# Optimization experiments

Hardware: AMD Instinct MI355X
Metric: run time of the kernel (lower is better)

The kernel has to match this reference:

```python
import jax, jax.numpy as jnp
import numpy as np

N_NODES = 50000
N_EDGES = 800000
N_GRAPHS = 256
NEG_SLOPE = 0.2

def selu(x):
    return jax.nn.selu(x)

def gat_conv(x, src, dst, W, att_l, att_r, b, n_nodes):
    """PyG GATConv, heads=1, with self-loops already appended to (src, dst).
    Message j->i: alpha_ij = softmax_i(leaky_relu(a_l.h_j + a_r.h_i)); out_i = sum_j alpha_ij h_j + b."""
    h = x @ W                                   # [N, C]
    a_src = h @ att_l                           # [N]
    a_dst = h @ att_r                           # [N]
    e = jax.nn.leaky_relu(a_src[src] + a_dst[dst], NEG_SLOPE)   # [E]
    # segment softmax over incoming edges of each dst node
    m = jax.ops.segment_max(e, dst, num_segments=n_nodes)       # [N]
    m = jnp.where(jnp.isfinite(m), m, 0.0)
    ex = jnp.exp(e - m[dst])
    denom = jax.ops.segment_sum(ex, dst, num_segments=n_nodes)  # [N]
    alpha = ex / jnp.maximum(denom, 1e-16)[dst]                  # [E]
    out = jax.ops.segment_sum(h[src] * alpha[:, None], dst, num_segments=n_nodes)
    return out + b

def global_mean_pool(x, batch, n_graphs):
    s = jax.ops.segment_sum(x, batch, num_segments=n_graphs)
    cnt = jax.ops.segment_sum(jnp.ones((x.shape[0],), x.dtype), batch, num_segments=n_graphs)
    return s / jnp.maximum(cnt, 1.0)[:, None]

def setup_inputs() -> dict:
    key = jax.random.key(0)
    ks = jax.random.split(key, 12)
    F_in, C, H, NC = 310, 256, 128, 2
    x = jax.random.normal(ks[0], (N_NODES, F_in), dtype=jnp.float32)
    edge_index = jax.random.randint(ks[1], (2, N_EDGES), 0, N_NODES, dtype=jnp.int64)
    batch = jnp.sort(jax.random.randint(ks[2], (N_NODES,), 0, N_GRAPHS, dtype=jnp.int64))
    g = lambda k, shp: jax.random.normal(k, shp, dtype=jnp.float32) * 0.05
    return {
        "x": x, "edge_index": edge_index, "batch": batch,
        "W1": g(ks[3], (F_in, C)), "att_l1": g(ks[4], (C,)), "att_r1": g(ks[5], (C,)),
        "b1": jnp.zeros((C,), jnp.float32),
        "W2": g(ks[6], (C, C)), "att_l2": g(ks[7], (C,)), "att_r2": g(ks[8], (C,)),
        "b2": jnp.zeros((C,), jnp.float32),
        "fc1_W": g(ks[9], (C, H)), "fc1_b": jnp.zeros((H,), jnp.float32),
        "fc2_W": g(ks[10], (H, NC)), "fc2_b": jnp.zeros((NC,), jnp.float32),
    }

def reference(x, edge_index, batch, W1, att_l1, att_r1, b1, W2, att_l2, att_r2, b2,
              fc1_W, fc1_b, fc2_W, fc2_b):
    n = x.shape[0]
    loops = jnp.arange(n, dtype=edge_index.dtype)
    src = jnp.concatenate([edge_index[0], loops])   # add_self_loops=True (PyG default)
    dst = jnp.concatenate([edge_index[1], loops])
    h = selu(gat_conv(x, src, dst, W1, att_l1, att_r1, b1, n))
    h = selu(gat_conv(h, src, dst, W2, att_l2, att_r2, b2, n))
    g = selu(global_mean_pool(h, batch, N_GRAPHS))      # [G, 256]
    g = selu(g @ fc1_W + fc1_b)                         # [G, 128]
    # dropout is identity in eval mode
    return jax.nn.log_softmax(g @ fc2_W + fc2_b, axis=-1)  # [G, 2]
```

## Files before the change

kernel.cpp:

```cpp
#include <hip/hip_runtime.h>
#include <hip/hip_bf16.h>

#define N_NODES 50000
#define N_EDGES 800000
#define N_TOT   (N_EDGES + N_NODES)
#define N_GRAPHS 256
#define F_IN 310
#define KP1 320
#define CH 256
#define HID 128
#define DEG_CAP 128

typedef __attribute__((ext_vector_type(8))) short short8;
typedef __attribute__((ext_vector_type(4))) float f32x4;
typedef unsigned short ushort_t;

__device__ __forceinline__ float selu_f(float x) {
    const float scale = 1.0507009873554805f;
    const float alpha = 1.6732632423543772f;
    return x > 0.f ? scale * x : scale * alpha * (expm1f(x));
}

__device__ __forceinline__ ushort_t f32_to_bf16_rne(float f) {
    unsigned u = __float_as_uint(f);
    unsigned rounding = 0x7FFFu + ((u >> 16) & 1u);
    return (ushort_t)((u + rounding) >> 16);
}
__device__ __forceinline__ float bf16_to_f32(ushort_t v) {
    return __uint_as_float(((unsigned)v) << 16);
}

__global__ __launch_bounds__(256) void convert_pad_x(
        const float* __restrict__ x, ushort_t* __restrict__ A) {
    int i = blockIdx.x * 256 + threadIdx.x;
    if (i >= N_NODES * (KP1 / 2)) return;
    int r = i / (KP1 / 2);
    int c2 = i - r * (KP1 / 2);
    int c = c2 * 2;
    ushort2 o = {0, 0};
    if (c2 < F_IN / 2) {
        float2 v = *(const float2*)(x + (long)r * F_IN + c);
        o.x = f32_to_bf16_rne(v.x);
        o.y = f32_to_bf16_rne(v.y);
    }
    *(ushort2*)(A + (long)r * KP1 + c) = o;
}

__global__ __launch_bounds__(256) void convert_wt(
        const float* __restrict__ W, ushort_t* __restrict__ Wt, int K, int Kp) {
    int i = blockIdx.x * blockDim.x + threadIdx.x;
    if (i >= CH * Kp) return;
    int n = i / Kp, k = i % Kp;
    Wt[i] = (k < K) ? f32_to_bf16_rne(W[(long)k * CH + n]) : 0;
}

__global__ __launch_bounds__(512) void gemm_bf16_fused(
        const ushort_t* __restrict__ A, const ushort_t* __restrict__ Bt,
        ushort_t* __restrict__ Cb, const float* __restrict__ att_l,
        const float* __restrict__ att_r, float* __restrict__ a_src,
        float* __restrict__ a_dst, int M, int Kp) {
    __shared__ __align__(16) ushort_t As[2][128 * 32];
    __shared__ __align__(16) ushort_t Bs[2][256 * 32];
    int tid = threadIdx.x;
    int row0 = blockIdx.x * 128;
    int w = tid >> 6, l = tid & 63;
    int lr = l & 15, lc = l >> 4;
    f32x4 acc[16] = {};

    int srow = l >> 2;
    int schunk = l & 3;
    int trowA = w * 16 + srow;
    int sx = schunk ^ (srow & 3);
    int garow = row0 + trowA; if (garow >= M) garow = M - 1;
    const ushort_t* gA  = A  + (size_t)garow * Kp + sx * 8;
    const ushort_t* gB0 = Bt + (size_t)trowA * Kp + sx * 8;
    const ushort_t* gB1 = Bt + (size_t)(128 + trowA) * Kp + sx * 8;
    int nt = Kp >> 5;

    auto stage = [&](int sel, int k0) {
        __builtin_amdgcn_global_load_lds(
            (const __attribute__((address_space(1))) void*)(gA + k0),
            (__attribute__((address_space(3))) void*)(&As[sel][w * 16 * 32]), 16, 0, 0);
        __builtin_amdgcn_global_load_lds(
            (const __attribute__((address_space(1))) void*)(gB0 + k0),
            (__attribute__((address_space(3))) void*)(&Bs[sel][w * 16 * 32]), 16, 0, 0);
        __builtin_amdgcn_global_load_lds(
            (const __attribute__((address_space(1))) void*)(gB1 + k0),
            (__attribute__((address_space(3))) void*)(&Bs[sel][(128 + w * 16) * 32]), 16, 0, 0);
    };

    stage(0, 0);
    __syncthreads();
    int cur = 0;
    for (int t = 0; t < nt; ++t) {
        if (t + 1 < nt) stage(cur ^ 1, (t + 1) << 5);
        int rA = w * 16 + lr;
        short8 af = *(const short8*)(&As[cur][rA * 32 + ((lc ^ (rA & 3)) * 8)]);
#pragma unroll
        for (int hn = 0; hn < 2; ++hn) {
            short8 bf[8];
#pragma unroll
            for (int nj = 0; nj < 8; ++nj) {
                int r = (hn * 8 + nj) * 16 + lr;
                bf[nj] = *(const short8*)(&Bs[cur][r * 32 + ((lc ^ (r & 3)) * 8)]);
            }
#pragma unroll
            for (int nj = 0; nj < 8; ++nj)
                acc[hn * 8 + nj] = __builtin_amdgcn_mfma_f32_16x16x32_bf16(
                    af, bf[nj], acc[hn * 8 + nj], 0, 0, 0);
        }
        __syncthreads();
        cur ^= 1;
    }

    float al[16], ar[16];
#pragma unroll
    for (int ni = 0; ni < 16; ++ni) {
        int col = ni * 16 + lr;
        al[ni] = att_l[col];
        ar[ni] = att_r[col];
    }
    int rbase = row0 + w * 16 + lc * 4;
#pragma unroll
    for (int q = 0; q < 4; ++q) {
        int grow = rbase + q;
        float pl = 0.f, pr = 0.f;
#pragma unroll
        for (int ni = 0; ni < 16; ++ni) {
            float v = acc[ni][q];
            pl += v * al[ni];
            pr += v * ar[ni];
            if (grow < M) Cb[(size_t)grow * CH + ni * 16 + lr] = f32_to_bf16_rne(v);
        }
#pragma unroll
        for (int off = 1; off < 16; off <<= 1) {
            pl += __shfl_xor(pl, off);
            pr += __shfl_xor(pr, off);
        }
        if (lr == 0 && grow < M) {
            a_src[grow] = pl;
            a_dst[grow] = pr;
        }
    }
}

__global__ __launch_bounds__(256) void deg_count(
        const int* __restrict__ ei, int* __restrict__ deg) {
    int eid = blockIdx.x * blockDim.x + threadIdx.x;
    if (eid >= N_TOT) return;
    int d = (eid < N_EDGES) ? ei[N_EDGES + eid] : eid - N_EDGES;
    atomicAdd(&deg[d], 1);
}

__global__ __launch_bounds__(256) void reserve_k(
        const int* __restrict__ deg, int* __restrict__ start,
        int* __restrict__ fillpos, int* __restrict__ cursor, int n) {
    int i = blockIdx.x * blockDim.x + threadIdx.x;
    if (i >= n) return;
    int s = atomicAdd(cursor, deg[i]);
    start[i] = s;
    fillpos[i] = s;
}

__global__ __launch_bounds__(256) void csr_fill(
        const int* __restrict__ ei, int* __restrict__ fillpos,
        int* __restrict__ csr_src) {
    int eid = blockIdx.x * blockDim.x + threadIdx.x;
    if (eid >= N_TOT) return;
    int s, d;
    if (eid < N_EDGES) { s = ei[eid]; d = ei[N_EDGES + eid]; }
    else { s = eid - N_EDGES; d = s; }
    int p = atomicAdd(&fillpos[d], 1);
    csr_src[p] = s;
}

__global__ __launch_bounds__(256) void gat_aggregate(
        const int* __restrict__ start, const int* __restrict__ deg,
        const int* __restrict__ csr_src,
        const float* __restrict__ a_src, const float* __restrict__ a_dst,
        const ushort_t* __restrict__ h, const float* __restrict__ bias,
        ushort_t* __restrict__ out_bf, int n) {
    __shared__ int   s_idx[4][DEG_CAP];
    __shared__ float s_ex[4][DEG_CAP];
    int wid = threadIdx.x >> 6;
    int lane = threadIdx.x & 63;
    int node = blockIdx.x * 4 + wid;
    if (node >= n) return;
    int s0 = start[node];
    int dg = deg[node];
    float ad = a_dst[node];
    bool cached = (dg <= DEG_CAP);

    float m = -1e30f;
    for (int i = lane; i < dg; i += 64) {
        int s = csr_src[s0 + i];
        float e = a_src[s] + ad;
        e = e > 0.f ? e : 0.2f * e;
        if (cached) { s_idx[wid][i] = s; s_ex[wid][i] = e; }
        m = fmaxf(m, e);
    }
#pragma unroll
    for (int off = 32; off > 0; off >>= 1) m = fmaxf(m, __shfl_xor(m, off));

    float sum = 0.f;
    if (cached) {
        for (int i = lane; i < dg; i += 64) {
            float ex = __expf(s_ex[wid][i] - m);
            s_ex[wid][i] = ex;
            sum += ex;
        }
    } else {
        for (int i = lane; i < dg; i += 64) {
            int s = csr_src[s0 + i];
            float e = a_src[s] + ad;
            e = e > 0.f ? e : 0.2f * e;
            sum += __expf(e - m);
        }
    }
#pragma unroll
    for (int off = 32; off > 0; off >>= 1) sum += __shfl_xor(sum, off);
    float inv = 1.f / fmaxf(sum, 1e-16f);

    float4 acc = {0.f, 0.f, 0.f, 0.f};
    if (cached) {
        int i = 0;
        for (; i + 4 <= dg; i += 4) {
            int sa = s_idx[wid][i],     sb = s_idx[wid][i + 1];
            int sc_ = s_idx[wid][i + 2], sd = s_idx[wid][i + 3];
            float xa = s_ex[wid][i] * inv,     xb = s_ex[wid][i + 1] * inv;
            float xc = s_ex[wid][i + 2] * inv, xd = s_ex[wid][i + 3] * inv;
            ushort4 ha = *(const ushort4*)(h + (long)sa * CH + lane * 4);
            ushort4 hb = *(const ushort4*)(h + (long)sb * CH + lane * 4);
            ushort4 hc = *(const ushort4*)(h + (long)sc_ * CH + lane * 4);
            ushort4 hd = *(const ushort4*)(h + (long)sd * CH + lane * 4);
            acc.x += xa * bf16_to_f32(ha.x) + xb * bf16_to_f32(hb.x)
                   + xc * bf16_to_f32(hc.x) + xd * bf16_to_f32(hd.x);
            acc.y += xa * bf16_to_f32(ha.y) + xb * bf16_to_f32(hb.y)
                   + xc * bf16_to_f32(hc.y) + xd * bf16_to_f32(hd.y);
            acc.z += xa * bf16_to_f32(ha.z) + xb * bf16_to_f32(hb.z)
                   + xc * bf16_to_f32(hc.z) + xd * bf16_to_f32(hd.z);
            acc.w += xa * bf16_to_f32(ha.w) + xb * bf16_to_f32(hb.w)
                   + xc * bf16_to_f32(hc.w) + xd * bf16_to_f32(hd.w);
        }
        for (; i < dg; i++) {
            int s = s_idx[wid][i];
            float xa = s_ex[wid][i] * inv;
            ushort4 hv = *(const ushort4*)(h + (long)s * CH + lane * 4);
            acc.x += xa * bf16_to_f32(hv.x);
            acc.y += xa * bf16_to_f32(hv.y);
            acc.z += xa * bf16_to_f32(hv.z);
            acc.w += xa * bf16_to_f32(hv.w);
        }
    } else {
        for (int i = 0; i < dg; i++) {
            int s = csr_src[s0 + i];
            float e = a_src[s] + ad;
            e = e > 0.f ? e : 0.2f * e;
            float alpha = __expf(e - m) * inv;
            ushort4 hv = *(const ushort4*)(h + (long)s * CH + lane * 4);
            acc.x += alpha * bf16_to_f32(hv.x);
            acc.y += alpha * bf16_to_f32(hv.y);
            acc.z += alpha * bf16_to_f32(hv.z);
            acc.w += alpha * bf16_to_f32(hv.w);
        }
    }
    float4 bv = *(const float4*)(bias + lane * 4);
    ushort4 ob;
    ob.x = f32_to_bf16_rne(selu_f(acc.x + bv.x));
    ob.y = f32_to_bf16_rne(selu_f(acc.y + bv.y));
    ob.z = f32_to_bf16_rne(selu_f(acc.z + bv.z));
    ob.w = f32_to_bf16_rne(selu_f(acc.w + bv.w));
    *(ushort4*)(out_bf + (long)node * CH + lane * 4) = ob;
}

__global__ __launch_bounds__(256) void pool_kernel(
        const ushort_t* __restrict__ h, const int* __restrict__ batch,
        float* __restrict__ g1) {
    int g = blockIdx.x;
    int t = threadIdx.x;
    int lo, hi;
    { int a = 0, b = N_NODES;
      while (a < b) { int mid = (a + b) >> 1; if (batch[mid] < g) a = mid + 1; else b = mid; }
      lo = a; }
    { int a = lo, b = N_NODES;
      while (a < b) { int mid = (a + b) >> 1; if (batch[mid] < g + 1) a = mid + 1; else b = mid; }
      hi = a; }
    float a0 = 0.f, a1 = 0.f, a2 = 0.f, a3 = 0.f;
    int i = lo;
    for (; i + 3 < hi; i += 4) {
        a0 += bf16_to_f32(h[(long)i * CH + t]);
        a1 += bf16_to_f32(h[(long)(i + 1) * CH + t]);
        a2 += bf16_to_f32(h[(long)(i + 2) * CH + t]);
        a3 += bf16_to_f32(h[(long)(i + 3) * CH + t]);
    }
    for (; i < hi; i++) a0 += bf16_to_f32(h[(long)i * CH + t]);
    float acc = (a0 + a1) + (a2 + a3);
    float cnt = (float)(hi - lo);
    g1[g * CH + t] = selu_f(acc / fmaxf(cnt, 1.f));
}

__global__ __launch_bounds__(128) void head_kernel(
        const float* __restrict__ g1, const float* __restrict__ fc1W,
        const float* __restrict__ fc1b, const float* __restrict__ fc2W,
        const float* __restrict__ fc2b, float* __restrict__ out) {
    __shared__ float row[CH];
    __shared__ float hrow[HID];
    __shared__ float logits[2];
    int g = blockIdx.x, t = threadIdx.x;
    row[t] = g1[g * CH + t];
    row[t + 128] = g1[g * CH + t + 128];
    __syncthreads();
    float acc = fc1b[t];
    for (int k = 0; k < CH; k++) acc += row[k] * fc1W[k * HID + t];
    hrow[t] = selu_f(acc);
    __syncthreads();
    if (t < 2) {
        float a = fc2b[t];
        for (int k = 0; k < HID; k++) a += hrow[k] * fc2W[k * 2 + t];
        logits[t] = a;
    }
    __syncthreads();
    if (t < 2) {
        float m = fmaxf(logits[0], logits[1]);
        float lse = logf(expf(logits[0] - m) + expf(logits[1] - m)) + m;
        out[g * 2 + t] = logits[t] - lse;
    }
}

extern "C" void kernel_launch(void* const* d_in, const int* in_sizes, int n_in,
                              void* d_out, int out_size, void* d_ws, size_t ws_size,
                              hipStream_t stream) {
    const float* x      = (const float*)d_in[0];
    const int*   ei     = (const int*)d_in[1];
    const int*   batch  = (const int*)d_in[2];
    const float* W1     = (const float*)d_in[3];
    const float* att_l1 = (const float*)d_in[4];
    const float* att_r1 = (const float*)d_in[5];
    const float* b1     = (const float*)d_in[6];
    const float* W2     = (const float*)d_in[7];
    const float* att_l2 = (const float*)d_in[8];
    const float* att_r2 = (const float*)d_in[9];
    const float* b2     = (const float*)d_in[10];
    const float* fc1W   = (const float*)d_in[11];
    const float* fc1b   = (const float*)d_in[12];
    const float* fc2W   = (const float*)d_in[13];
    const float* fc2b   = (const float*)d_in[14];
    float* out = (float*)d_out;

    char* ws = (char*)d_ws;
    size_t off = 0;
    auto alloc = [&](size_t bytes) {
        void* p = ws + off;
        off += (bytes + 255) & ~(size_t)255;
        return p;
    };
    ushort_t* Ab     = (ushort_t*)alloc((size_t)N_NODES * KP1 * 2);
    ushort_t* Hb1    = (ushort_t*)alloc((size_t)N_NODES * CH * 2);
    ushort_t* Zb2    = (ushort_t*)alloc((size_t)N_NODES * CH * 2);
    ushort_t* Hb2    = (ushort_t*)alloc((size_t)N_NODES * CH * 2);
    ushort_t* W1t    = (ushort_t*)alloc((size_t)CH * KP1 * 2);
    ushort_t* W2t    = (ushort_t*)alloc((size_t)CH * CH * 2);
    float*    a_src  = (float*)alloc((size_t)N_NODES * 4);
    float*    a_dst  = (float*)alloc((size_t)N_NODES * 4);
    int*      deg    = (int*)alloc((size_t)N_NODES * 4);
    int*      startA = (int*)alloc((size_t)N_NODES * 4);
    int*      fillpos= (int*)alloc((size_t)N_NODES * 4);
    int*      csr_src= (int*)alloc((size_t)N_TOT * 4);
    int*      cursor = (int*)alloc(256);
    float*    g1     = (float*)alloc((size_t)N_GRAPHS * CH * 4);

    dim3 blk(256);
    int gemm_grid = (N_NODES + 127) / 128;
    int conv_grid = (N_NODES * (KP1 / 2) + 255) / 256;
    int edge_grid = (N_TOT + 255) / 256;
    int node_grid = (N_NODES + 255) / 256;
    int agg_grid  = (N_NODES + 3) / 4;

    convert_pad_x<<<conv_grid, blk, 0, stream>>>(x, Ab);
    convert_wt<<<(CH * KP1 + 255) / 256, blk, 0, stream>>>(W1, W1t, F_IN, KP1);
    convert_wt<<<(CH * CH + 255) / 256, blk, 0, stream>>>(W2, W2t, CH, CH);
    hipMemsetAsync(deg, 0, (size_t)N_NODES * 4, stream);
    hipMemsetAsync(cursor, 0, 4, stream);
    deg_count<<<edge_grid, blk, 0, stream>>>(ei, deg);
    reserve_k<<<node_grid, blk, 0, stream>>>(deg, startA, fillpos, cursor, N_NODES);
    csr_fill<<<edge_grid, blk, 0, stream>>>(ei, fillpos, csr_src);

    gemm_bf16_fused<<<gemm_grid, dim3(512), 0, stream>>>(Ab, W1t, Hb1, att_l1, att_r1,
                                                         a_src, a_dst, N_NODES, KP1);
    gat_aggregate<<<agg_grid, blk, 0, stream>>>(startA, deg, csr_src, a_src, a_dst,
                                                Hb1, b1, Zb2, N_NODES);

    gemm_bf16_fused<<<gemm_grid, dim3(512), 0, stream>>>(Zb2, W2t, Hb2, att_l2, att_r2,
                                                         a_src, a_dst, N_NODES, CH);
    gat_aggregate<<<agg_grid, blk, 0, stream>>>(startA, deg, csr_src, a_src, a_dst,
                                                Hb2, b2, Hb1, N_NODES);

    pool_kernel<<<N_GRAPHS, blk, 0, stream>>>(Hb1, batch, g1);
    head_kernel<<<N_GRAPHS, dim3(128), 0, stream>>>(g1, fc1W, fc1b, fc2W, fc2b, out);
}
```

Baseline: 325.7 us.

## Retile GEMM to 2x4 wave grid and drop max pass in segment softmax

Result: no change. 329.9 us (+1.3%).

```diff
diff --git a/kernel.cpp b/kernel.cpp
--- a/kernel.cpp
+++ b/kernel.cpp
@@ -61,11 +61,13 @@
         float* __restrict__ a_dst, int M, int Kp) {
     __shared__ __align__(16) ushort_t As[2][128 * 32];
     __shared__ __align__(16) ushort_t Bs[2][256 * 32];
+    __shared__ float s_pl[128], s_pr[128];
     int tid = threadIdx.x;
     int row0 = blockIdx.x * 128;
     int w = tid >> 6, l = tid & 63;
     int lr = l & 15, lc = l >> 4;
-    f32x4 acc[16] = {};
+    int wr = w >> 2, wc = w & 3;
+    f32x4 acc[4][4] = {};
 
     int srow = l >> 2;
     int schunk = l & 3;
@@ -94,53 +96,66 @@
     int cur = 0;
     for (int t = 0; t < nt; ++t) {
         if (t + 1 < nt) stage(cur ^ 1, (t + 1) << 5);
-        int rA = w * 16 + lr;
-        short8 af = *(const short8*)(&As[cur][rA * 32 + ((lc ^ (rA & 3)) * 8)]);
-#pragma unroll
-        for (int hn = 0; hn < 2; ++hn) {
-            short8 bf[8];
-#pragma unroll
-            for (int nj = 0; nj < 8; ++nj) {
-                int r = (hn * 8 + nj) * 16 + lr;
-                bf[nj] = *(const short8*)(&Bs[cur][r * 32 + ((lc ^ (r & 3)) * 8)]);
-            }
-#pragma unroll
-            for (int nj = 0; nj < 8; ++nj)
-                acc[hn * 8 + nj] = __builtin_amdgcn_mfma_f32_16x16x32_bf16(
-                    af, bf[nj], acc[hn * 8 + nj], 0, 0, 0);
-        }
+        short8 af[4], bf[4];
+#pragma unroll
+        for (int mi = 0; mi < 4; ++mi) {
+            int r = wr * 64 + mi * 16 + lr;
+            af[mi] = *(const short8*)(&As[cur][r * 32 + ((lc ^ (r & 3)) * 8)]);
+        }
+#pragma unroll
+        for (int ni = 0; ni < 4; ++ni) {
+            int r = wc * 64 + ni * 16 + lr;
+            bf[ni] = *(const short8*)(&Bs[cur][r * 32 + ((lc ^ (r & 3)) * 8)]);
+        }
+#pragma unroll
+        for (int mi = 0; mi < 4; ++mi)
+#pragma unroll
+            for (int ni = 0; ni < 4; ++ni)
+                acc[mi][ni] = __builtin_amdgcn_mfma_f32_16x16x32_bf16(
+                    af[mi], bf[ni], acc[mi][ni], 0, 0, 0);
         __syncthreads();
         cur ^= 1;
     }
 
-    float al[16], ar[16];
-#pragma unroll
-    for (int ni = 0; ni < 16; ++ni) {
-        int col = ni * 16 + lr;
+    if (tid < 128) { s_pl[tid] = 0.f; s_pr[tid] = 0.f; }
+    __syncthreads();
+    float al[4], ar[4];
+#pragma unroll
+    for (int ni = 0; ni < 4; ++ni) {
+        int col = wc * 64 + ni * 16 + lr;
         al[ni] = att_l[col];
         ar[ni] = att_r[col];
     }
-    int rbase = row0 + w * 16 + lc * 4;
-#pragma unroll
-    for (int q = 0; q < 4; ++q) {
-        int grow = rbase + q;
-        float pl = 0.f, pr = 0.f;
-#pragma unroll
-        for (int ni = 0; ni < 16; ++ni) {
-            float v = acc[ni][q];
-            pl += v * al[ni];
-            pr += v * ar[ni];
-            if (grow < M) Cb[(size_t)grow * CH + ni * 16 + lr] = f32_to_bf16_rne(v);
-        }
-#pragma unroll
-        for (int off = 1; off < 16; off <<= 1) {
-            pl += __shfl_xor(pl, off);
-            pr += __shfl_xor(pr, off);
-        }
-        if (lr == 0 && grow < M) {
-            a_src[grow] = pl;
-            a_dst[grow] = pr;
-        }
+#pragma unroll
+    for (int mi = 0; mi < 4; ++mi) {
+        int lrow = wr * 64 + mi * 16 + lc * 4;
+#pragma unroll
+        for (int q = 0; q < 4; ++q) {
+            int grow = row0 + lrow + q;
+            float pl = 0.f, pr = 0.f;
+#pragma unroll
+            for (int ni = 0; ni < 4; ++ni) {
+                float v = acc[mi][ni][q];
+                pl += v * al[ni];
+                pr += v * ar[ni];
+                if (grow < M)
+                    Cb[(size_t)grow * CH + wc * 64 + ni * 16 + lr] = f32_to_bf16_rne(v);
+            }
+#pragma unroll
+            for (int off = 1; off < 16; off <<= 1) {
+                pl += __shfl_xor(pl, off);
+                pr += __shfl_xor(pr, off);
+            }
+            if (lr == 0) {
+                atomicAdd(&s_pl[lrow + q], pl);
+                atomicAdd(&s_pr[lrow + q], pr);
+            }
+        }
+    }
+    __syncthreads();
+    if (tid < 128 && row0 + tid < M) {
+        a_src[row0 + tid] = s_pl[tid];
+        a_dst[row0 + tid] = s_pr[tid];
     }
 }
 
@@ -191,31 +206,14 @@
     float ad = a_dst[node];
     bool cached = (dg <= DEG_CAP);
 
-    float m = -1e30f;
+    float sum = 0.f;
     for (int i = lane; i < dg; i += 64) {
         int s = csr_src[s0 + i];
         float e = a_src[s] + ad;
-        e = e > 0.f ? e : 0.2f * e;
-        if (cached) { s_idx[wid][i] = s; s_ex[wid][i] = e; }
-        m = fmaxf(m, e);
-    }
-#pragma unroll
-    for (int off = 32; off > 0; off >>= 1) m = fmaxf(m, __shfl_xor(m, off));
-
-    float sum = 0.f;
-    if (cached) {
-        for (int i = lane; i < dg; i += 64) {
-            float ex = __expf(s_ex[wid][i] - m);
-            s_ex[wid][i] = ex;
-            sum += ex;
-        }
-    } else {
-        for (int i = lane; i < dg; i += 64) {
-            int s = csr_src[s0 + i];
-            float e = a_src[s] + ad;
-            e = e > 0.f ? e : 0.2f * e;
-            sum += __expf(e - m);
-        }
+        e = fmaxf(e, 0.2f * e);
+        float ex = __expf(e);
+        if (cached) { s_idx[wid][i] = s; s_ex[wid][i] = ex; }
+        sum += ex;
     }
 #pragma unroll
     for (int off = 32; off > 0; off >>= 1) sum += __shfl_xor(sum, off);
@@ -255,8 +253,8 @@
         for (int i = 0; i < dg; i++) {
             int s = csr_src[s0 + i];
             float e = a_src[s] + ad;
-            e = e > 0.f ? e : 0.2f * e;
-            float alpha = __expf(e - m) * inv;
+            e = fmaxf(e, 0.2f * e);
+            float alpha = __expf(e) * inv;
             ushort4 hv = *(const ushort4*)(h + (long)s * CH + lane * 4);
             acc.x += alpha * bf16_to_f32(hv.x);
             acc.y += alpha * bf16_to_f32(hv.y);
```
